# Kernel tuning notes

Hardware: AMD Instinct MI355X
Metric: run time of the kernel (lower is better)

Reference implementation:

```python
import jax, jax.numpy as jnp
import numpy as np

N_FFT = 4096
HOP = 1024
EPS = 1e-10


def hann(n):
    # periodic Hann window, matches torch.hann_window(n)
    return 0.5 - 0.5 * jnp.cos(2.0 * jnp.pi * jnp.arange(n) / n)


def stft(x, window):
    # x: (..., T) real -> (..., F, frames) complex; center=True, reflect pad, onesided
    pad = N_FFT // 2
    x = jnp.pad(x, [(0, 0)] * (x.ndim - 1) + [(pad, pad)], mode='reflect')
    n_frames = 1 + (x.shape[-1] - N_FFT) // HOP
    idx = jnp.arange(n_frames)[:, None] * HOP + jnp.arange(N_FFT)[None, :]
    frames = x[..., idx] * window  # (..., frames, N_FFT)
    return jnp.swapaxes(jnp.fft.rfft(frames, axis=-1), -1, -2)  # (..., F, frames)


def istft(spec, window, length):
    # spec: (..., F, frames) complex -> (..., length) real; torch.istft semantics (center=True)
    frames = jnp.fft.irfft(jnp.swapaxes(spec, -1, -2), n=N_FFT, axis=-1) * window
    n_frames = frames.shape[-2]
    out_len = N_FFT + HOP * (n_frames - 1)
    idx = (jnp.arange(n_frames)[:, None] * HOP + jnp.arange(N_FFT)[None, :]).reshape(-1)
    flat = frames.reshape(frames.shape[:-2] + (-1,))
    y = jnp.zeros(frames.shape[:-2] + (out_len,), frames.dtype).at[..., idx].add(flat)
    wsq = jnp.zeros((out_len,), frames.dtype).at[idx].add(jnp.tile(window ** 2, n_frames))
    y = y / jnp.where(wsq > 1e-11, wsq, 1.0)
    pad = N_FFT // 2
    return y[..., pad:pad + length]


def setup_inputs() -> dict:
    key = jax.random.key(0)
    k1, k2, k3 = jax.random.split(key, 3)
    audio = jax.random.normal(k1, (2, 2, 441000), jnp.float32)
    W = jax.random.normal(k2, (4, 2049, 2049), jnp.float32) * 0.02
    b = jax.random.normal(k3, (4, 2049), jnp.float32) * 0.01
    return {"audio": audio, "W": W, "b": b}


def reference(audio, W, b):
    window = hann(N_FFT).astype(audio.dtype)
    mix = stft(audio, window)                 # (N, C, F, T) complex64
    X = jnp.abs(mix)                          # ComplexNorm, mono=False, power=1
    Xd = jax.lax.stop_gradient(X)             # Separator feeds X.detach() to target models
    # target models: per-target linear over frequency bins + ReLU (nonneg spectrogram)
    V = jax.nn.relu(jnp.einsum('ncft,jgf->njcgt', Xd, W) + b[None, :, None, :, None])
    # wiener(iterations=0, softmask=False, residual=False): y_j = v_j * exp(i*angle(mix))
    phase = mix / (jnp.abs(mix) + EPS)        # unit-magnitude complex
    Y = V.astype(phase.real.dtype) * phase[:, None]  # (N, J, C, F, T) complex
    estimates = istft(Y, window, audio.shape[-1])    # (N, J, C, T_audio)
    return estimates
```

## Files before the change

### kernel.cpp

```cpp
#include <hip/hip_runtime.h>
#include <hip/hip_bf16.h>
#include <math.h>

#define T_AUDIO 441000
#define NH   2048
#define HOP  1024
#define NBINS 2049
#define NFRAMES 431
#define PAD  2048

#define GP  2176
#define KP  2112
#define TPN 448

#define NBLK 108
#define SPAN 7168

#define NSTFT (4 * NFRAMES)
#define NCONV ((4 * GP * KP / 8 + 255) / 256)
#define NPREP (NSTFT + NCONV + 4)

#define TWO_PI 6.2831853071795864769f

#define PADI(i) ((i) + ((i) >> 4))

typedef __bf16 bf16_t;
typedef bf16_t bf16x8 __attribute__((ext_vector_type(8)));
typedef bf16_t bf16x4 __attribute__((ext_vector_type(4)));
typedef float f32x4 __attribute__((ext_vector_type(4)));
typedef float f32x4u __attribute__((ext_vector_type(4), aligned(4)));
typedef _Float16 h16;
typedef h16 h16x2 __attribute__((ext_vector_type(2)));

__device__ __forceinline__ unsigned pack_bf2(float a, float b) {
    union { bf16_t h; unsigned short u; } ca, cb;
    ca.h = (bf16_t)a; cb.h = (bf16_t)b;
    return (unsigned)ca.u | ((unsigned)cb.u << 16);
}
__device__ __forceinline__ float2 unpack_bf2(unsigned v) {
    union { unsigned u; float f; } a, b;
    a.u = v << 16;
    b.u = v & 0xffff0000u;
    return make_float2(a.f, b.f);
}

__device__ __forceinline__ float2 cadd(float2 a, float2 b) { return make_float2(a.x + b.x, a.y + b.y); }
__device__ __forceinline__ float2 csub(float2 a, float2 b) { return make_float2(a.x - b.x, a.y - b.y); }
__device__ __forceinline__ float2 cmul(float2 a, float2 b) {
    return make_float2(a.x * b.x - a.y * b.y, a.x * b.y + a.y * b.x);
}
__device__ __forceinline__ float2 cmulc(float2 u, float2 w) {
    return make_float2(u.x * w.x + u.y * w.y, u.y * w.x - u.x * w.y);
}

__global__ void k_tab(float2* __restrict__ tw) {
    int i = blockIdx.x * 256 + threadIdx.x;
    if (i < 4096) {
        float s, c;
        sincosf((float)i * (TWO_PI / 4096.0f), &s, &c);
        tw[i] = make_float2(c, s);
    }
}


__device__ __forceinline__ void load_own(float2 v[8], const float2* x, int tid) {
    #pragma unroll
    for (int k = 0; k < 8; k++) v[k] = x[PADI(tid + 256 * k)];
}

template<bool FWD>
__device__ __forceinline__ void r8_sweep_store(const float2 v[8], float2* x,
        int tid, int s, int ls, int fac, const float2* __restrict__ tw) {
    const float sgn = FWD ? -1.0f : 1.0f;
    const float R2 = 0.70710678118654752440f;
    int q = tid & (s - 1);
    int p = tid >> ls;
    int e = p * fac;
    float2 w[7];
    #pragma unroll
    for (int k = 0; k < 7; k++) w[k] = tw[e * (k + 1)];
    float2 s0 = cadd(v[0], v[4]), s1 = cadd(v[1], v[5]),
           s2 = cadd(v[2], v[6]), s3 = cadd(v[3], v[7]);
    float2 d0 = csub(v[0], v[4]), d1 = csub(v[1], v[5]),
           d2 = csub(v[2], v[6]), d3 = csub(v[3], v[7]);
    float2 X0, X1, X2, X3, X4, X5, X6, X7;
    {
        float2 t0 = cadd(s0, s2), t1 = csub(s0, s2);
        float2 t2 = cadd(s1, s3), t3 = csub(s1, s3);
        float2 it3 = make_float2(-sgn * t3.y, sgn * t3.x);
        X0 = cadd(t0, t2); X4 = csub(t0, t2);
        X2 = cadd(t1, it3); X6 = csub(t1, it3);
    }
    {
        float2 e0 = d0;
        float2 e1 = make_float2(R2 * (d1.x - sgn * d1.y), R2 * (sgn * d1.x + d1.y));
        float2 e2 = make_float2(-sgn * d2.y, sgn * d2.x);
        float2 e3 = make_float2(-R2 * (d3.x + sgn * d3.y), R2 * (sgn * d3.x - d3.y));
        float2 t0 = cadd(e0, e2), t1 = csub(e0, e2);
        float2 t2 = cadd(e1, e3), t3 = csub(e1, e3);
        float2 it3 = make_float2(-sgn * t3.y, sgn * t3.x);
        X1 = cadd(t0, t2); X5 = csub(t0, t2);
        X3 = cadd(t1, it3); X7 = csub(t1, it3);
    }
    int ob = q + 8 * s * p;
    x[PADI(ob)] = X0;
    float2 XX[7] = {X1, X2, X3, X4, X5, X6, X7};
    #pragma unroll
    for (int k = 0; k < 7; k++) {
        float2 u = XX[k];
        x[PADI(ob + s * (k + 1))] = FWD ? cmulc(u, w[k]) : cmul(w[k], u);
    }
}

__device__ __forceinline__ void r4_final_reg(const float2 v[8], float2 o[8],
                                             float sgn) {
    #pragma unroll
    for (int h = 0; h < 2; h++) {
        float2 c0 = v[h], c1 = v[h + 2], c2 = v[h + 4], c3 = v[h + 6];
        float2 t0 = cadd(c0, c2), t1 = csub(c0, c2);
        float2 t2 = cadd(c1, c3), t3 = csub(c1, c3);
        float2 it3 = make_float2(-sgn * t3.y, sgn * t3.x);
        o[h]     = cadd(t0, t2);
        o[h + 2] = cadd(t1, it3);
        o[h + 4] = csub(t0, t2);
        o[h + 6] = csub(t1, it3);
    }
}

template<bool FWD>
__device__ __forceinline__ void fft_mid(float2 v[8], float2* buf, int tid,
                                        const float2* __restrict__ tw) {
    r8_sweep_store<FWD>(v, buf, tid, 1, 0, 2, tw);
    __syncthreads();
    load_own(v, buf, tid);
    __syncthreads();
    r8_sweep_store<FWD>(v, buf, tid, 8, 3, 16, tw);
    __syncthreads();
    load_own(v, buf, tid);
    __syncthreads();
    r8_sweep_store<FWD>(v, buf, tid, 64, 6, 128, tw);
    __syncthreads();
    load_own(v, buf, tid);
    __syncthreads();
}

__global__ __launch_bounds__(256) void k_prep(const float* __restrict__ audio,
        const float* __restrict__ W, bf16_t* __restrict__ Wb,
        bf16_t* __restrict__ Xb, unsigned* __restrict__ ph,
        const float2* __restrict__ tw) {
    __shared__ float2 buf[2176];
    int bid = blockIdx.x;
    int tid = threadIdx.x;
    if (bid >= NSTFT) {
        if (bid >= NSTFT + NCONV) {
            int nc = bid - NSTFT - NCONV;
            bf16_t* dst = Xb + ((size_t)nc * TPN + NFRAMES) * KP;
            bf16x8 z = {};
            for (int i = tid; i < (TPN - NFRAMES) * KP / 8; i += 256)
                *(bf16x8*)(dst + (size_t)i * 8) = z;
            return;
        }
        size_t idx = (size_t)(bid - NSTFT) * 256 + tid;
        size_t total = (size_t)4 * GP * KP / 8;
        if (idx >= total) return;
        size_t e = idx * 8;
        int f0 = (int)(e % KP);
        size_t rem = e / KP;
        int g = (int)(rem % GP);
        int j = (int)(rem / GP);
        bf16x8 v = {};
        if (g < NBINS) {
            const float* src = W + ((size_t)j * NBINS + g) * NBINS;
            if (f0 + 7 < NBINS) {
                f32x4u a0 = *(const f32x4u*)(src + f0);
                f32x4u a1 = *(const f32x4u*)(src + f0 + 4);
                #pragma unroll
                for (int r = 0; r < 4; r++) { v[r] = (bf16_t)a0[r]; v[r + 4] = (bf16_t)a1[r]; }
            } else {
                #pragma unroll
                for (int r = 0; r < 8; r++) {
                    int f = f0 + r;
                    v[r] = (bf16_t)(f < NBINS ? src[f] : 0.0f);
                }
            }
        }
        *(bf16x8*)(Wb + e) = v;
        return;
    }
    int nc = bid / NFRAMES;
    int fr = bid - nc * NFRAMES;
    const float* a = audio + (size_t)nc * T_AUDIO;
    int base = fr * HOP - PAD;
    float2 v[8];
    #pragma unroll
    for (int it = 0; it < 8; it++) {
        int m = tid + it * 256;
        float4 tt = ((const float4*)tw)[m];
        float w0 = 0.5f - 0.5f * tt.x, w1 = 0.5f - 0.5f * tt.z;
        int x0 = base + 2 * m;
        if (x0 >= 0 && x0 + 1 < T_AUDIO) {
            float2 av = *(const float2*)(a + x0);
            v[it] = make_float2(av.x * w0, av.y * w1);
        } else {
            int r0 = x0, r1 = x0 + 1;
            r0 = r0 < 0 ? -r0 : (r0 >= T_AUDIO ? 2 * T_AUDIO - 2 - r0 : r0);
            r1 = r1 < 0 ? -r1 : (r1 >= T_AUDIO ? 2 * T_AUDIO - 2 - r1 : r1);
            v[it] = make_float2(a[r0] * w0, a[r1] * w1);
        }
    }
    fft_mid<true>(v, buf, tid, tw);
    {
        float2 o[8];
        r4_final_reg(v, o, -1.0f);
        #pragma unroll
        for (int it = 0; it < 8; it++) buf[PADI(tid + 256 * it)] = o[it];
    }
    __syncthreads();
    size_t orow = ((size_t)nc * NFRAMES + fr) * KP;
    bf16_t* Xrow = Xb + ((size_t)nc * TPN + fr) * KP;
    for (int k = tid; k < NBINS; k += 256) {
        float2 Zk = buf[PADI(k & 2047)];
        float2 Zm = buf[PADI((2048 - k) & 2047)];
        float ex = 0.5f * (Zk.x + Zm.x), ey = 0.5f * (Zk.y - Zm.y);
        float ox = 0.5f * (Zk.y + Zm.y), oy = -0.5f * (Zk.x - Zm.x);
        float2 w = tw[k];
        float re = ex + w.x * ox + w.y * oy;
        float im = ey + w.x * oy - w.y * ox;
        float mag = sqrtf(re * re + im * im);
        float inv = 1.0f / (mag + 1e-10f);
        Xrow[k] = (bf16_t)mag;
        ph[orow + k] = pack_bf2(re * inv, im * inv);
    }
    for (int k = NBINS + tid; k < KP; k += 256) Xrow[k] = (bf16_t)0.0f;
}

__global__ __launch_bounds__(256) void k_gemm_mfma(const bf16_t* __restrict__ Wb,
        const float* __restrict__ bias, const bf16_t* __restrict__ Xb,
        bf16_t* __restrict__ V) {
    __shared__ bf16_t As[128 * 64];
    __shared__ bf16_t Bs[64 * 64];
    int id = blockIdx.x;
    int xcd = id & 7, nn = id >> 3;
    int G = xcd + 8 * (nn / 28);
    if (G >= 68) return;
    int m28 = nn % 28;
    int j  = G / 17;
    int g0 = (G % 17) * 128;
    int nc = m28 / 7;
    int t0 = (m28 % 7) * 64;
    const bf16_t* A = Wb + ((size_t)j * GP + g0) * KP;
    const bf16_t* B = Xb + ((size_t)nc * TPN + t0) * KP;
    int tid = threadIdx.x;
    int lane = tid & 63, wid = tid >> 6;
    int wm = wid >> 1, wn = wid & 1;

    const bf16_t* srcA[4];
    #pragma unroll
    for (int i = 0; i < 4; i++) {
        int s = i * 256 + tid;
        int r = s >> 3, cc = (s & 7) ^ (r & 7);
        srcA[i] = A + (size_t)r * KP + cc * 8;
    }
    const bf16_t* srcB[2];
    #pragma unroll
    for (int i = 0; i < 2; i++) {
        int s = i * 256 + tid;
        int r = s >> 3, cc = (s & 7) ^ (r & 7);
        srcB[i] = B + (size_t)r * KP + cc * 8;
    }

    int laneLo = lane & 15, laneHi = lane >> 4;
    int offA[4][2], offB[2][2];
    #pragma unroll
    for (int mm = 0; mm < 4; mm++) {
        int r = wm * 64 + mm * 16 + laneLo;
        #pragma unroll
        for (int kk = 0; kk < 2; kk++) {
            int c = kk * 4 + laneHi;
            offA[mm][kk] = r * 128 + ((c ^ (r & 7)) << 4);
        }
    }
    #pragma unroll
    for (int n = 0; n < 2; n++) {
        int r = wn * 32 + n * 16 + laneLo;
        #pragma unroll
        for (int kk = 0; kk < 2; kk++) {
            int c = kk * 4 + laneHi;
            offB[n][kk] = r * 128 + ((c ^ (r & 7)) << 4);
        }
    }

    f32x4 acc[4][2];
    #pragma unroll
    for (int mm = 0; mm < 4; mm++)
        #pragma unroll
        for (int n = 0; n < 2; n++)
            acc[mm][n] = (f32x4){0.f, 0.f, 0.f, 0.f};

    for (int k0 = 0; k0 < KP; k0 += 64) {
        #pragma unroll
        for (int i = 0; i < 4; i++)
            __builtin_amdgcn_global_load_lds(
                (const __attribute__((address_space(1))) void*)(srcA[i] + k0),
                (__attribute__((address_space(3))) void*)(As + (i * 256 + tid) * 8),
                16, 0, 0);
        #pragma unroll
        for (int i = 0; i < 2; i++)
            __builtin_amdgcn_global_load_lds(
                (const __attribute__((address_space(1))) void*)(srcB[i] + k0),
                (__attribute__((address_space(3))) void*)(Bs + (i * 256 + tid) * 8),
                16, 0, 0);
        __syncthreads();

        bf16x8 af[4][2], bfr[2][2];
        #pragma unroll
        for (int mm = 0; mm < 4; mm++)
            #pragma unroll
            for (int kk = 0; kk < 2; kk++)
                af[mm][kk] = *(const bf16x8*)((const char*)As + offA[mm][kk]);
        #pragma unroll
        for (int n = 0; n < 2; n++)
            #pragma unroll
            for (int kk = 0; kk < 2; kk++)
                bfr[n][kk] = *(const bf16x8*)((const char*)Bs + offB[n][kk]);
        #pragma unroll
        for (int mm = 0; mm < 4; mm++)
            #pragma unroll
            for (int n = 0; n < 2; n++)
                #pragma unroll
                for (int kk = 0; kk < 2; kk++)
                    acc[mm][n] = __builtin_amdgcn_mfma_f32_16x16x32_bf16(
                        af[mm][kk], bfr[n][kk], acc[mm][n], 0, 0, 0);
        __syncthreads();
    }

    int jnc = j * 4 + nc;
    int colT = laneLo;
    int rowB = laneHi * 4;
    #pragma unroll
    for (int n = 0; n < 2; n++) {
        int t = t0 + wn * 32 + n * 16 + colT;
        if (t >= NFRAMES) continue;
        size_t vrow = ((size_t)jnc * NFRAMES + t) * KP;
        #pragma unroll
        for (int mm = 0; mm < 4; mm++) {
            int g = g0 + wm * 64 + mm * 16 + rowB;
            if (g + 3 < NBINS) {
                bf16x4 o;
                #pragma unroll
                for (int r = 0; r < 4; r++)
                    o[r] = (bf16_t)fmaxf(acc[mm][n][r] + bias[j * NBINS + g + r], 0.0f);
                *(bf16x4*)(V + vrow + g) = o;
            } else {
                #pragma unroll
                for (int r = 0; r < 4; r++) {
                    int gg = g + r;
                    if (gg < NBINS)
                        V[vrow + gg] = (bf16_t)fmaxf(acc[mm][n][r] + bias[j * NBINS + gg], 0.0f);
                }
            }
        }
    }
}

__global__ __launch_bounds__(256) void k_istft(const bf16_t* __restrict__ V,
        const unsigned* __restrict__ ph, const float2* __restrict__ tw,
        h16* __restrict__ strips) {
    __shared__ float2 buf[2176];
    __shared__ __align__(16) unsigned char stg[12336];
    bf16_t*   Vs = (bf16_t*)stg;
    unsigned* Ps = (unsigned*)(stg + 4112);
    int id = blockIdx.x;
    int xcd = id & 7, slot = id >> 3;
    int wgid = xcd * 216 + slot;
    int j = wgid & 3;
    int t4 = wgid >> 2;
    int nc = t4 / NBLK;
    int b  = t4 - nc * NBLK;
    int njc = (nc >> 1) * 8 + j * 2 + (nc & 1);
    int jnc = j * 4 + nc;
    int tid = threadIdx.x;
    const float scale = 1.0f / 2048.0f;
    float2 acc[14];
    #pragma unroll
    for (int u = 0; u < 14; u++) acc[u] = make_float2(0.f, 0.f);

#define STAGE_F(fr_)                                                           \
    {                                                                          \
        const bf16_t* vsrc = V + ((size_t)jnc * NFRAMES + (fr_)) * KP;         \
        const unsigned* psrc = ph + ((size_t)nc * NFRAMES + (fr_)) * KP;       \
        __builtin_amdgcn_global_load_lds(                                      \
            (const __attribute__((address_space(1))) void*)(vsrc + tid * 8),   \
            (__attribute__((address_space(3))) void*)(Vs + tid * 8), 16, 0, 0);\
        __builtin_amdgcn_global_load_lds(                                      \
            (const __attribute__((address_space(1))) void*)(psrc + tid * 4),   \
            (__attribute__((address_space(3))) void*)(Ps + tid * 4), 16, 0, 0);\
        __builtin_amdgcn_global_load_lds(                                      \
            (const __attribute__((address_space(1))) void*)(psrc + 1024 + tid * 4), \
            (__attribute__((address_space(3))) void*)(Ps + 1024 + tid * 4), 16, 0, 0); \
        if (tid == 0) {                                                        \
            __builtin_amdgcn_global_load_lds(                                  \
                (const __attribute__((address_space(1))) void*)(vsrc + 2048),  \
                (__attribute__((address_space(3))) void*)(Vs + 2048), 16, 0, 0); \
            __builtin_amdgcn_global_load_lds(                                  \
                (const __attribute__((address_space(1))) void*)(psrc + 2048),  \
                (__attribute__((address_space(3))) void*)(Ps + 2048), 16, 0, 0); \
        }                                                                      \
    }

    STAGE_F(b * 4);
    __syncthreads();

    #pragma unroll
    for (int p = 0; p < 4; p++) {
        int fr = b * 4 + p;
        if (fr < NFRAMES) {
            float2 v[8];
            #pragma unroll
            for (int it = 0; it < 8; it++) {
                int k = tid + it * 256;
                int km = 2048 - k;
                float vk = (float)Vs[k];
                float2 pk = unpack_bf2(Ps[k]);
                float vm = (float)Vs[km];
                float2 pm = unpack_bf2(Ps[km]);
                float2 Yk = make_float2(vk * pk.x, vk * pk.y);
                float2 Ym = make_float2(vm * pm.x, vm * pm.y);
                float ex = 0.5f * (Yk.x + Ym.x), ey = 0.5f * (Yk.y - Ym.y);
                float wx = 0.5f * (Yk.x - Ym.x), wy = 0.5f * (Yk.y + Ym.y);
                float2 w = tw[k];
                float ox_ = w.x * wx - w.y * wy;
                float oy_ = w.x * wy + w.y * wx;
                v[it] = make_float2(ex - oy_, ey + ox_);
            }
            __syncthreads();
            if (p < 3) STAGE_F(fr + 1);
            fft_mid<false>(v, buf, tid, tw);
            float2 o[8];
            r4_final_reg(v, o, 1.0f);
            #pragma unroll
            for (int it = 0; it < 8; it++) {
                int m = tid + it * 256;
                float4 tt = ((const float4*)tw)[m];
                acc[2 * p + it].x += o[it].x * scale * (0.5f - 0.5f * tt.x);
                acc[2 * p + it].y += o[it].y * scale * (0.5f - 0.5f * tt.z);
            }
        }
    }
#undef STAGE_F
    h16* dst = strips + ((size_t)njc * NBLK + b) * SPAN;
    #pragma unroll
    for (int u = 0; u < 14; u++) {
        h16x2 o = { (h16)acc[u].x, (h16)acc[u].y };
        *(h16x2*)(dst + 512 * u + 2 * tid) = o;
    }
}

__global__ __launch_bounds__(256) void k_final(const h16* __restrict__ strips,
        const float2* __restrict__ tw, float* __restrict__ out) {
    int gidx = blockIdx.x * 256 + threadIdx.x;
    int t = gidx * 2;
    if (t >= T_AUDIO) return;
    int njc = blockIdx.y;
    const h16* S = strips + (size_t)njc * NBLK * SPAN;
    float o[2];
    #pragma unroll
    for (int u = 0; u < 2; u++) {
        int tt = t + u;
        int q = tt + PAD;
        int b1 = q >> 12, o1 = q & 4095;
        float s = 0.f;
        if (b1 < NBLK) s += (float)S[b1 * SPAN + o1];
        if (b1 > 0 && o1 < SPAN - 4096) s += (float)S[(b1 - 1) * SPAN + o1 + 4096];
        float wsq;
        if (tt >= 1024 && tt <= 439295) {
            wsq = 1.5f;
        } else {
            wsq = 0.f;
            int ib = q >> 10;
            #pragma unroll
            for (int d = 0; d < 4; d++) {
                int i = ib - d;
                if (i >= 0 && i < NFRAMES) {
                    int m = q - (i << 10);
                    float w = 0.5f - 0.5f * tw[m].x;
                    wsq += w * w;
                }
            }
            if (!(wsq > 1e-11f)) wsq = 1.f;
        }
        o[u] = s / wsq;
    }
    *(float2*)(out + (size_t)njc * T_AUDIO + t) = make_float2(o[0], o[1]);
}

extern "C" void kernel_launch(void* const* d_in, const int* in_sizes, int n_in,
                              void* d_out, int out_size, void* d_ws, size_t ws_size,
                              hipStream_t stream) {
    const float* audio = (const float*)d_in[0];
    const float* Wm    = (const float*)d_in[1];
    const float* bias  = (const float*)d_in[2];
    float* out = (float*)d_out;
    char* ws = (char*)d_ws;

    size_t szWb  = (size_t)4 * GP * KP * sizeof(bf16_t);
    size_t szXb  = (size_t)4 * TPN * KP * sizeof(bf16_t);
    size_t szPh  = (size_t)4 * NFRAMES * KP * sizeof(unsigned);
    size_t szV   = (size_t)16 * NFRAMES * KP * sizeof(bf16_t);
    size_t szStr = (size_t)16 * NBLK * SPAN * sizeof(h16);
    size_t szTw  = (size_t)4096 * sizeof(float2);

    bf16_t*   Wb    = (bf16_t*)ws;   ws += szWb;
    bf16_t*   Xb    = (bf16_t*)ws;   ws += szXb;
    unsigned* ph    = (unsigned*)ws; ws += szPh;
    bf16_t*   V     = (bf16_t*)ws;   ws += szV;
    h16*      strips= (h16*)ws;      ws += szStr;
    float2*   tw    = (float2*)ws;   ws += szTw;
    if ((size_t)(ws - (char*)d_ws) > ws_size) return;

    k_tab<<<dim3(16), 256, 0, stream>>>(tw);
    k_prep<<<dim3(NPREP), 256, 0, stream>>>(audio, Wm, Wb, Xb, ph, tw);
    k_gemm_mfma<<<dim3(72 * 28), 256, 0, stream>>>(Wb, bias, Xb, V);
    k_istft<<<dim3(1728), 256, 0, stream>>>(V, ph, tw, strips);
    k_final<<<dim3((T_AUDIO / 2 + 255) / 256, 16), 256, 0, stream>>>(strips, tw, out);
}
```

Before: 206.6 us.

## Double-buffer GEMM LDS tiles with K=32 stages and async prefetch

Splits the GEMM K-loop into 32-wide stages held in two LDS buffers and issues the global-to-LDS loads for stage t+2 while stage t is being computed. Explicit vmcnt waits replace full syncthreads, with a new 4-column XOR swizzle to fit the narrower tile. The aim is to hide global load latency behind MFMA work. In exchange there are twice as many barriers per unit of K, and each stage carries only half the MFMA work, which may leave too little compute to cover the latency.

```diff
diff --git a/kernel.cpp b/kernel.cpp
--- a/kernel.cpp
+++ b/kernel.cpp
@@ -12,6 +12,7 @@
 #define GP  2176
 #define KP  2112
 #define TPN 448
+#define NKT2 66
 
 #define NBLK 108
 #define SPAN 7168
@@ -237,8 +238,8 @@
 __global__ __launch_bounds__(256) void k_gemm_mfma(const bf16_t* __restrict__ Wb,
         const float* __restrict__ bias, const bf16_t* __restrict__ Xb,
         bf16_t* __restrict__ V) {
-    __shared__ bf16_t As[128 * 64];
-    __shared__ bf16_t Bs[64 * 64];
+    __shared__ bf16_t As[2][128 * 32];
+    __shared__ bf16_t Bs[2][64 * 32];
     int id = blockIdx.x;
     int xcd = id & 7, nn = id >> 3;
     int G = xcd + 8 * (nn / 28);
@@ -254,40 +255,45 @@
     int lane = tid & 63, wid = tid >> 6;
     int wm = wid >> 1, wn = wid & 1;
 
-    const bf16_t* srcA[4];
-    #pragma unroll
-    for (int i = 0; i < 4; i++) {
-        int s = i * 256 + tid;
-        int r = s >> 3, cc = (s & 7) ^ (r & 7);
-        srcA[i] = A + (size_t)r * KP + cc * 8;
-    }
-    const bf16_t* srcB[2];
+    const bf16_t* srcA[2];
     #pragma unroll
     for (int i = 0; i < 2; i++) {
         int s = i * 256 + tid;
-        int r = s >> 3, cc = (s & 7) ^ (r & 7);
-        srcB[i] = B + (size_t)r * KP + cc * 8;
+        int r = s >> 2, cc = (s & 3) ^ ((r >> 2) & 3);
+        srcA[i] = A + (size_t)r * KP + cc * 8;
+    }
+    const bf16_t* srcB0;
+    {
+        int s = tid;
+        int r = s >> 2, cc = (s & 3) ^ ((r >> 2) & 3);
+        srcB0 = B + (size_t)r * KP + cc * 8;
+    }
+
+#define STAGE(bufsel, koff)                                                    \
+    {                                                                          \
+        _Pragma("unroll")                                                      \
+        for (int i = 0; i < 2; i++)                                            \
+            __builtin_amdgcn_global_load_lds(                                  \
+                (const __attribute__((address_space(1))) void*)(srcA[i] + (koff)), \
+                (__attribute__((address_space(3))) void*)(&As[bufsel][(i * 256 + tid) * 8]), \
+                16, 0, 0);                                                     \
+        __builtin_amdgcn_global_load_lds(                                      \
+            (const __attribute__((address_space(1))) void*)(srcB0 + (koff)),   \
+            (__attribute__((address_space(3))) void*)(&Bs[bufsel][tid * 8]),   \
+            16, 0, 0);                                                         \
     }
 
     int laneLo = lane & 15, laneHi = lane >> 4;
-    int offA[4][2], offB[2][2];
+    int offA[4], offB[2];
     #pragma unroll
     for (int mm = 0; mm < 4; mm++) {
         int r = wm * 64 + mm * 16 + laneLo;
-        #pragma unroll
-        for (int kk = 0; kk < 2; kk++) {
-            int c = kk * 4 + laneHi;
-            offA[mm][kk] = r * 128 + ((c ^ (r & 7)) << 4);
-        }
+        offA[mm] = r * 64 + ((laneHi ^ ((r >> 2) & 3)) << 4);
     }
     #pragma unroll
     for (int n = 0; n < 2; n++) {
         int r = wn * 32 + n * 16 + laneLo;
-        #pragma unroll
-        for (int kk = 0; kk < 2; kk++) {
-            int c = kk * 4 + laneHi;
-            offB[n][kk] = r * 128 + ((c ^ (r & 7)) << 4);
-        }
+        offB[n] = r * 64 + ((laneHi ^ ((r >> 2) & 3)) << 4);
     }
 
     f32x4 acc[4][2];
@@ -297,42 +303,33 @@
         for (int n = 0; n < 2; n++)
             acc[mm][n] = (f32x4){0.f, 0.f, 0.f, 0.f};
 
-    for (int k0 = 0; k0 < KP; k0 += 64) {
-        #pragma unroll
-        for (int i = 0; i < 4; i++)
-            __builtin_amdgcn_global_load_lds(
-                (const __attribute__((address_space(1))) void*)(srcA[i] + k0),
-                (__attribute__((address_space(3))) void*)(As + (i * 256 + tid) * 8),
-                16, 0, 0);
-        #pragma unroll
-        for (int i = 0; i < 2; i++)
-            __builtin_amdgcn_global_load_lds(
-                (const __attribute__((address_space(1))) void*)(srcB[i] + k0),
-                (__attribute__((address_space(3))) void*)(Bs + (i * 256 + tid) * 8),
-                16, 0, 0);
-        __syncthreads();
-
-        bf16x8 af[4][2], bfr[2][2];
+    STAGE(0, 0);
+    STAGE(1, 32);
+    for (int t = 0; t < NKT2; ++t) {
+        if (t == NKT2 - 1) asm volatile("s_waitcnt vmcnt(0)" ::: "memory");
+        else               asm volatile("s_waitcnt vmcnt(3)" ::: "memory");
+        __builtin_amdgcn_s_barrier();
+
+        const char* aB = (const char*)&As[t & 1][0];
+        const char* bB = (const char*)&Bs[t & 1][0];
+        bf16x8 af[4], bfr[2];
         #pragma unroll
         for (int mm = 0; mm < 4; mm++)
-            #pragma unroll
-            for (int kk = 0; kk < 2; kk++)
-                af[mm][kk] = *(const bf16x8*)((const char*)As + offA[mm][kk]);
+            af[mm] = *(const bf16x8*)(aB + offA[mm]);
         #pragma unroll
         for (int n = 0; n < 2; n++)
-            #pragma unroll
-            for (int kk = 0; kk < 2; kk++)
-                bfr[n][kk] = *(const bf16x8*)((const char*)Bs + offB[n][kk]);
+            bfr[n] = *(const bf16x8*)(bB + offB[n]);
         #pragma unroll
         for (int mm = 0; mm < 4; mm++)
             #pragma unroll
             for (int n = 0; n < 2; n++)
-                #pragma unroll
-                for (int kk = 0; kk < 2; kk++)
-                    acc[mm][n] = __builtin_amdgcn_mfma_f32_16x16x32_bf16(
-                        af[mm][kk], bfr[n][kk], acc[mm][n], 0, 0, 0);
-        __syncthreads();
-    }
+                acc[mm][n] = __builtin_amdgcn_mfma_f32_16x16x32_bf16(
+                    af[mm], bfr[n], acc[mm][n], 0, 0, 0);
+
+        __builtin_amdgcn_s_barrier();
+        if (t + 2 < NKT2) STAGE(t & 1, (t + 2) * 32);
+    }
+#undef STAGE
 
     int jnc = j * 4 + nc;
     int colT = laneLo;
```

Result: slower. 236.1 us (+14.2%).
